# Kernel optimization log

Measured on AMD Instinct MI355X. Metric: run time of the kernel, lower is better.

## Reference

```python
import jax, jax.numpy as jnp
import numpy as np

N_HEAD = 16
HEAD_DIM = 128  # n_embd // n_head
RMS_EPS = 1.1920929e-07  # torch.finfo(float32).eps, F.rms_norm default
ROPE_BASE = 10000.0


def _rope_tables(T, head_dim, dtype=jnp.float32):
    half = head_dim // 2
    inv_freq = 1.0 / (ROPE_BASE ** (jnp.arange(half, dtype=jnp.float32) / half))
    t = jnp.arange(T, dtype=jnp.float32)
    freqs = jnp.outer(t, inv_freq)  # [T, half]
    return jnp.cos(freqs).astype(dtype), jnp.sin(freqs).astype(dtype)


def _apply_rope(x, cos, sin):
    # x: [B, T, H, D]; cos/sin: [T, D//2]
    half = x.shape[-1] // 2
    x1, x2 = x[..., :half], x[..., half:]
    c = cos[None, :, None, :]
    s = sin[None, :, None, :]
    return jnp.concatenate([x1 * c - x2 * s, x1 * s + x2 * c], axis=-1)


def _rms_norm(x):
    ms = jnp.mean(jnp.square(x), axis=-1, keepdims=True)
    return x * jax.lax.rsqrt(ms + RMS_EPS)


def setup_inputs() -> dict:
    key = jax.random.key(0)
    ks = jax.random.split(key, 5)
    B, T, E = 4, 2048, 2048
    x = jax.random.normal(ks[0], (B, T, E), dtype=jnp.float32)
    scale = 0.02
    wq = jax.random.normal(ks[1], (E, E), dtype=jnp.float32) * scale
    wk = jax.random.normal(ks[2], (E, E), dtype=jnp.float32) * scale
    wv = jax.random.normal(ks[3], (E, E), dtype=jnp.float32) * scale
    wo = jax.random.normal(ks[4], (E, E), dtype=jnp.float32) * scale
    return {"x": x, "wq": wq, "wk": wk, "wv": wv, "wo": wo}


def reference(x, wq, wk, wv, wo):
    B, T, E = x.shape
    H, D = N_HEAD, HEAD_DIM
    # QKV projections (bias-free linears)
    q = (x @ wq).reshape(B, T, H, D)
    k = (x @ wk).reshape(B, T, H, D)
    v = (x @ wv).reshape(B, T, H, D)
    # RoPE then parameter-free QK RMS norm
    cos, sin = _rope_tables(T, D, x.dtype)
    q = _rms_norm(_apply_rope(q, cos, sin))
    k = _rms_norm(_apply_rope(k, cos, sin))
    # causal SDPA
    scale = 1.0 / jnp.sqrt(jnp.asarray(D, dtype=x.dtype))
    scores = jnp.einsum('bqhd,bkhd->bhqk', q, k) * scale
    causal = jnp.tril(jnp.ones((T, T), dtype=bool))
    scores = jnp.where(causal[None, None], scores, jnp.asarray(-jnp.inf, scores.dtype))
    attn = jax.nn.softmax(scores, axis=-1)
    y = jnp.einsum('bhqk,bkhd->bqhd', attn, v).reshape(B, T, E)
    return y @ wo
```

## Files before the change

kernel.cpp:

```cpp
#include <hip/hip_runtime.h>
#include <math.h>

#define T_SEQ 2048
#define BATCH 4
#define E_DIM 2048
#define NHEAD 16
#define HDIM 128
#define RMS_EPS 1.1920929e-07f
#define NQT (T_SEQ / 128)

typedef unsigned short u16;
typedef __attribute__((ext_vector_type(8))) unsigned short u16x8;
typedef __attribute__((ext_vector_type(8))) short bf16x8;
typedef __attribute__((ext_vector_type(4))) float f32x4;

typedef const __attribute__((address_space(1))) unsigned int g_u32;
typedef __attribute__((address_space(3))) unsigned int l_u32;

static __device__ __forceinline__ u16 f2b(float f) {
  unsigned int u = __builtin_bit_cast(unsigned int, f);
  u += 0x7fffu + ((u >> 16) & 1u);
  return (u16)(u >> 16);
}
static __device__ __forceinline__ float b2f(u16 v) {
  return __builtin_bit_cast(float, ((unsigned int)v) << 16);
}

__global__ __launch_bounds__(256) void convert_f32_bf16(
    const float* __restrict__ src, u16* __restrict__ dst, int n) {
  int i = (blockIdx.x * 256 + threadIdx.x) * 4;
  if (i >= n) return;
  float4 v = *reinterpret_cast<const float4*>(src + i);
  ushort4 o;
  o.x = f2b(v.x); o.y = f2b(v.y); o.z = f2b(v.z); o.w = f2b(v.w);
  *reinterpret_cast<ushort4*>(dst + i) = o;
}

__global__ __launch_bounds__(256) void convt_w_k(
    const float* __restrict__ W, u16* __restrict__ Wt) {
  __shared__ u16 tile[64][72];
  int c0 = blockIdx.x * 64;
  int r0 = blockIdx.y * 64;
  int tid = threadIdx.x;
  int lrow = tid >> 2;
  int lcol = (tid & 3) * 16;
#pragma unroll
  for (int i = 0; i < 4; ++i) {
    float4 v = *reinterpret_cast<const float4*>(
        W + (long long)(r0 + lrow) * E_DIM + c0 + lcol + i * 4);
    tile[lrow][lcol + i * 4 + 0] = f2b(v.x);
    tile[lrow][lcol + i * 4 + 1] = f2b(v.y);
    tile[lrow][lcol + i * 4 + 2] = f2b(v.z);
    tile[lrow][lcol + i * 4 + 3] = f2b(v.w);
  }
  __syncthreads();
  int wrow = tid >> 2;
  int wcol = (tid & 3) * 16;
  u16 o[16];
#pragma unroll
  for (int i = 0; i < 16; ++i) o[i] = tile[wcol + i][wrow];
  u16* dst = Wt + (long long)(c0 + wrow) * E_DIM + r0 + wcol;
  *reinterpret_cast<u16x8*>(dst)     = *reinterpret_cast<u16x8*>(&o[0]);
  *reinterpret_cast<u16x8*>(dst + 8) = *reinterpret_cast<u16x8*>(&o[8]);
}

__global__ __launch_bounds__(256) void rope_tables_k(
    float* __restrict__ cost, float* __restrict__ sint) {
  int idx = blockIdx.x * 256 + threadIdx.x;
  int i = idx & 63, t = idx >> 6;
  double inv = pow(10000.0, -(double)i / 64.0);
  double ang = (double)t * inv;
  cost[idx] = (float)cos(ang);
  sint[idx] = (float)sin(ang);
}

__global__ __launch_bounds__(256) void rope_rms_k(
    u16* __restrict__ Qb, u16* __restrict__ Kb, const float* __restrict__ cost,
    const float* __restrict__ sint) {
  int half = gridDim.x >> 1;
  int isK = blockIdx.x >= half;
  u16* qk = isK ? Kb : Qb;
  float outscale = isK ? 1.0f : 0.08838834764831845f;
  int wave = threadIdx.x >> 6;
  int lane = threadIdx.x & 63;
  long long row = (long long)(blockIdx.x - (isK ? half : 0)) * 4 + wave;
  int th = (int)(row >> 4);
  int t = th & (T_SEQ - 1);
  u16* p = qk + row * HDIM;
  float x1 = b2f(p[lane]);
  float x2 = b2f(p[lane + 64]);
  float c = cost[t * 64 + lane];
  float s = sint[t * 64 + lane];
  float o1 = x1 * c - x2 * s;
  float o2 = x1 * s + x2 * c;
  float ss = o1 * o1 + o2 * o2;
#pragma unroll
  for (int m = 32; m >= 1; m >>= 1) ss += __shfl_xor(ss, m, 64);
  float r = rsqrtf(ss * (1.0f / 128.0f) + RMS_EPS) * outscale;
  p[lane] = f2b(o1 * r);
  p[lane + 64] = f2b(o2 * r);
}

__global__ __launch_bounds__(256) void transpose_v_k(
    const u16* __restrict__ V, u16* __restrict__ Vt) {
  __shared__ u16 tile[64][72];
  int t0 = blockIdx.x * 64, d0 = blockIdx.y * 64;
  int bh = blockIdx.z;
  int b = bh >> 4, h = bh & 15;
  int tid = threadIdx.x;
  int lrow = tid >> 3;
  int lcol = (tid & 7) * 8;
#pragma unroll
  for (int pass = 0; pass < 2; ++pass) {
    int row = lrow + pass * 32;
    const u16* src = V + ((((long long)b * T_SEQ + t0 + row) * NHEAD + h) << 7) + d0 + lcol;
    *reinterpret_cast<u16x8*>(&tile[row][lcol]) = *reinterpret_cast<const u16x8*>(src);
  }
  __syncthreads();
#pragma unroll
  for (int pass = 0; pass < 2; ++pass) {
    int drow = (tid >> 3) + pass * 32;
    int tcol = (tid & 7) * 8;
    u16x8 o;
#pragma unroll
    for (int i = 0; i < 8; ++i) o[i] = tile[tcol + i][drow];
    u16* dst = Vt + ((long long)bh * HDIM + d0 + drow) * T_SEQ + t0 + tcol;
    *reinterpret_cast<u16x8*>(dst) = o;
  }
}

__global__ __launch_bounds__(512, 2) void gemm_bt_k(
    const u16* __restrict__ A,
    const u16* __restrict__ Bt0, const u16* __restrict__ Bt1, const u16* __restrict__ Bt2,
    u16* __restrict__ C0, u16* __restrict__ C1, u16* __restrict__ C2,
    float* __restrict__ Cf, int M, int N, int K) {
  int lin = blockIdx.x + (blockIdx.y << 3) + (blockIdx.z << 8);
  int kx = lin & 7, ii = lin >> 3;
  int by = ((kx >> 1) << 3) + (ii & 7);
  int bx, bz;
  if (gridDim.z == 3) {
    int u = (kx & 1) * 12 + (ii >> 3);
    bx = u & 7; bz = u >> 3;
  } else {
    bx = ((kx & 1) << 2) + (ii >> 3);
    bz = 0;
  }
  const u16* Bt = bz == 0 ? Bt0 : (bz == 1 ? Bt1 : Bt2);
  u16* C = bz == 0 ? C0 : (bz == 1 ? C1 : C2);

  __shared__ u16 As[2][256 * 64];
  __shared__ u16 Bs[2][256 * 64];
  u16* A0 = As[0]; u16* A1 = As[1];
  u16* B0 = Bs[0]; u16* B1 = Bs[1];
  const int tid = threadIdx.x;
  const int lane = tid & 63, wave = tid >> 6;
  const int wm = wave >> 2, wn = wave & 3;
  const int m0 = by * 256, n0 = bx * 256;
  const int lr = lane & 15, lq = lane >> 4, l7 = lane & 7;
  const int NT = K >> 6;

  int rowA[2][2], rowB[2][2];
  const u16* gA[2][2];
  const u16* gB[2][2];
#pragma unroll
  for (int l = 0; l < 2; ++l) {
    int rihb = l * 64 + wave * 8;
#pragma unroll
    for (int h = 0; h < 2; ++h) {
      int ra = ((rihb >> 6) << 7) + h * 64 + (rihb & 63);
      int rb = ((rihb >> 5) << 6) + h * 32 + (rihb & 31);
      rowA[h][l] = ra;
      rowB[h][l] = rb;
      int rA = ra + (lane >> 3);
      int rB = rb + (lane >> 3);
      gA[h][l] = A + (long long)(m0 + rA) * K + ((l7 ^ (rA & 7)) * 8);
      gB[h][l] = Bt + (long long)(n0 + rB) * K + ((l7 ^ (rB & 7)) * 8);
    }
  }

  f32x4 acc[8][4] = {};
  bf16x8 aX[2][2], aY[2][2], bB[4][2];

#define GLDS(gp, lp) \
  __builtin_amdgcn_global_load_lds((g_u32*)(gp), (l_u32*)(lp), 16, 0, 0)
#define STG_A(bufp, h, off) do {                                              \
    GLDS(gA[h][0] + (off), (bufp) + rowA[h][0] * 64);                         \
    GLDS(gA[h][1] + (off), (bufp) + rowA[h][1] * 64); } while (0)
#define STG_B(bufp, h, off) do {                                              \
    GLDS(gB[h][0] + (off), (bufp) + rowB[h][0] * 64);                         \
    GLDS(gB[h][1] + (off), (bufp) + rowB[h][1] * 64); } while (0)
#define LDSA(dst, buf, mtb)                                                   \
  _Pragma("unroll") for (int mi = 0; mi < 2; ++mi)                            \
  _Pragma("unroll") for (int ks = 0; ks < 2; ++ks)                            \
    dst[mi][ks] = *reinterpret_cast<const bf16x8*>(                           \
        (buf) + (wm * 128 + ((mtb) + mi) * 16 + lr) * 64 +                    \
        ((((ks) << 2) + lq) ^ l7) * 8);
#define LDSB(dst, buf)                                                        \
  _Pragma("unroll") for (int ni = 0; ni < 4; ++ni)                            \
  _Pragma("unroll") for (int ks = 0; ks < 2; ++ks)                            \
    dst[ni][ks] = *reinterpret_cast<const bf16x8*>(                           \
        (buf) + (wn * 64 + (ni) * 16 + lr) * 64 +                             \
        ((((ks) << 2) + lq) ^ l7) * 8);
#define MFMA2(ph, a)                                                          \
  _Pragma("unroll") for (int mi = 0; mi < 2; ++mi)                            \
  _Pragma("unroll") for (int ni = 0; ni < 4; ++ni)                            \
  _Pragma("unroll") for (int ks = 0; ks < 2; ++ks)                            \
    acc[(ph) * 2 + mi][ni] = __builtin_amdgcn_mfma_f32_16x16x32_bf16(         \
        a[mi][ks], bB[ni][ks], acc[(ph) * 2 + mi][ni], 0, 0, 0);
#define SB __builtin_amdgcn_sched_barrier(0)
#define BAR __builtin_amdgcn_s_barrier()
#define VMC(n) asm volatile("s_waitcnt vmcnt(" #n ")" ::: "memory")
#define PH_MID SB; BAR; SB; __builtin_amdgcn_s_setprio(1)
#define PH_END __builtin_amdgcn_s_setprio(0); SB

  GLDS(gB[0][0], B0 + rowB[0][0] * 64); GLDS(gB[0][1], B0 + rowB[0][1] * 64);
  GLDS(gB[1][0], B0 + rowB[1][0] * 64); GLDS(gB[1][1], B0 + rowB[1][1] * 64);
  GLDS(gA[0][0], A0 + rowA[0][0] * 64); GLDS(gA[0][1], A0 + rowA[0][1] * 64);
  GLDS(gA[1][0], A0 + rowA[1][0] * 64); GLDS(gA[1][1], A0 + rowA[1][1] * 64);
  GLDS(gB[0][0] + 64, B1 + rowB[0][0] * 64); GLDS(gB[0][1] + 64, B1 + rowB[0][1] * 64);
  GLDS(gB[1][0] + 64, B1 + rowB[1][0] * 64); GLDS(gB[1][1] + 64, B1 + rowB[1][1] * 64);
  GLDS(gA[0][0] + 64, A1 + rowA[0][0] * 64); GLDS(gA[0][1] + 64, A1 + rowA[0][1] * 64);
  VMC(6);
  BAR; SB;
  LDSB(bB, B0);
  LDSA(aX, A0, 0);
  SB;

#pragma unroll 1
  for (int t = 0; t < NT; t += 2) {
    const bool nl = (t + 2 < NT);
    LDSA(aY, A0, 2);
    STG_A(A1, 1, 64);
    PH_MID; MFMA2(0, aX); PH_END;
    LDSA(aX, A0, 4);
    if (nl) { STG_B(B0, 0, 128); VMC(6); } else { VMC(4); }
    PH_MID; MFMA2(1, aY); PH_END;
    LDSA(aY, A0, 6);
    if (nl) { STG_B(B0, 1, 128); VMC(4); } else { VMC(0); }
    PH_MID; MFMA2(2, aX); PH_END;
    LDSA(aX, A1, 0);
    if (nl) STG_A(A0, 0, 128);
    PH_MID; MFMA2(3, aY);
    LDSB(bB, B1);
    PH_END;
    LDSA(aY, A1, 2);
    if (nl) STG_A(A0, 1, 128);
    PH_MID; MFMA2(0, aX); PH_END;
    LDSA(aX, A1, 4);
    if (nl) { STG_B(B1, 0, 192); VMC(6); }
    PH_MID; MFMA2(1, aY); PH_END;
    LDSA(aY, A1, 6);
    if (nl) { STG_B(B1, 1, 192); VMC(4); }
    PH_MID; MFMA2(2, aX); PH_END;
    LDSA(aX, A0, 0);
    if (nl) STG_A(A1, 0, 192);
    PH_MID; MFMA2(3, aY);
    LDSB(bB, B0);
    PH_END;
#pragma unroll
    for (int l = 0; l < 2; ++l)
#pragma unroll
      for (int h = 0; h < 2; ++h) { gA[h][l] += 128; gB[h][l] += 128; }
  }
#undef LDSA
#undef LDSB
#undef MFMA2
#undef STG_A
#undef STG_B
#undef GLDS
#undef PH_MID
#undef PH_END

#pragma unroll
  for (int mt = 0; mt < 8; ++mt)
#pragma unroll
    for (int nt = 0; nt < 4; ++nt) {
      long long col = n0 + wn * 64 + nt * 16 + lr;
#pragma unroll
      for (int r = 0; r < 4; ++r) {
        long long row = m0 + wm * 128 + mt * 16 + lq * 4 + r;
        float v = acc[mt][nt][r];
        if (Cf) Cf[row * N + col] = v;
        else C[row * N + col] = f2b(v);
      }
    }
}

__global__ __launch_bounds__(256, 3) void attn_k(
    const u16* __restrict__ Q, const u16* __restrict__ K,
    const u16* __restrict__ Vt, u16* __restrict__ Y) {
  __shared__ u16 Ks[64 * 128];
  __shared__ u16 Vs[128 * 64];
  __shared__ u16 Ps[4][32 * 72];
  __shared__ float Al[4][32];
  int lin = blockIdx.x + (blockIdx.y << 3);
  int pair = (lin >> 6);
  int bh = ((lin & 7) << 3) + ((lin >> 3) & 7);
  int b = bh >> 4, h = bh & 15;
  int tid = threadIdx.x, lane = tid & 63, wave = tid >> 6;
  int lr = lane & 15, lq = lane >> 4;

  const u16* kp[4];
  const u16* vp[4];
#pragma unroll
  for (int p = 0; p < 4; ++p) {
    int c = p * 256 + wave * 64 + lane;
    int key = c >> 4, sk = c & 15, gk = (sk - key) & 15;
    kp[p] = K + (((long long)b * T_SEQ + key) * NHEAD + h) * HDIM + gk * 8;
    int d = c >> 3, sv = c & 7, gv = (sv - d) & 7;
    vp[p] = Vt + ((long long)bh * HDIM + d) * T_SEQ + gv * 8;
  }

#pragma unroll 1
  for (int phase = 0; phase < 2; ++phase) {
    int qt = phase == 0 ? (NQT - 1 - pair) : pair;
    int qbase = qt * 128 + wave * 32;

    bf16x8 aq[2][4];
#pragma unroll
    for (int n2 = 0; n2 < 2; ++n2) {
      const u16* qp = Q + (((long long)b * T_SEQ + qbase + n2 * 16 + lr) * NHEAD + h) * HDIM;
#pragma unroll
      for (int kt = 0; kt < 4; ++kt)
        aq[n2][kt] = *reinterpret_cast<const bf16x8*>(qp + kt * 32 + lq * 8);
    }

    float m_s[2], l_s[2];
#pragma unroll
    for (int n2 = 0; n2 < 2; ++n2) { m_s[n2] = -INFINITY; l_s[n2] = 0.f; }
    f32x4 o[2][8] = {};

    int niter = 2 * qt + 2;
    for (int j = 0; j < niter; ++j) {
      __syncthreads();
#pragma unroll
      for (int p = 0; p < 4; ++p) {
        __builtin_amdgcn_global_load_lds(
            (g_u32*)(kp[p] + (long long)j * 64 * NHEAD * HDIM),
            (l_u32*)(Ks + p * 2048 + wave * 512), 16, 0, 0);
        __builtin_amdgcn_global_load_lds(
            (g_u32*)(vp[p] + j * 64),
            (l_u32*)(Vs + p * 2048 + wave * 512), 16, 0, 0);
      }
      __syncthreads();

      f32x4 s[4][2];
#pragma unroll
      for (int mt = 0; mt < 4; ++mt) {
        int key = mt * 16 + lr;
        bf16x8 ak[4];
#pragma unroll
        for (int kt = 0; kt < 4; ++kt) {
          int slot = (kt * 4 + lq + key) & 15;
          ak[kt] = *reinterpret_cast<const bf16x8*>(&Ks[key * 128 + slot * 8]);
        }
#pragma unroll
        for (int n2 = 0; n2 < 2; ++n2) {
          f32x4 acc = {};
#pragma unroll
          for (int kt = 0; kt < 4; ++kt)
            acc = __builtin_amdgcn_mfma_f32_16x16x32_bf16(ak[kt], aq[n2][kt], acc, 0, 0, 0);
          s[mt][n2] = acc;
        }
      }

      if (j >= 2 * qt) {
#pragma unroll
        for (int mt = 0; mt < 4; ++mt)
#pragma unroll
          for (int n2 = 0; n2 < 2; ++n2) {
            int q = qbase + n2 * 16 + lr;
#pragma unroll
            for (int r = 0; r < 4; ++r) {
              int key = j * 64 + mt * 16 + lq * 4 + r;
              if (key > q) s[mt][n2][r] = -INFINITY;
            }
          }
      }

      float alpha[2];
#pragma unroll
      for (int n2 = 0; n2 < 2; ++n2) {
        float mx = s[0][n2][0];
#pragma unroll
        for (int mt = 0; mt < 4; ++mt)
#pragma unroll
          for (int r = 0; r < 4; ++r) mx = fmaxf(mx, s[mt][n2][r]);
        mx = fmaxf(mx, __shfl_xor(mx, 16, 64));
        mx = fmaxf(mx, __shfl_xor(mx, 32, 64));
        float mn = fmaxf(m_s[n2], mx);
        alpha[n2] = __expf(m_s[n2] - mn);
        m_s[n2] = mn;
        float sum = 0.f;
        int q = n2 * 16 + lr;
#pragma unroll
        for (int mt = 0; mt < 4; ++mt) {
          ushort4 pk;
          float p0 = __expf(s[mt][n2][0] - mn);
          float p1 = __expf(s[mt][n2][1] - mn);
          float p2 = __expf(s[mt][n2][2] - mn);
          float p3 = __expf(s[mt][n2][3] - mn);
          sum += (p0 + p1) + (p2 + p3);
          pk.x = f2b(p0); pk.y = f2b(p1); pk.z = f2b(p2); pk.w = f2b(p3);
          *reinterpret_cast<ushort4*>(&Ps[wave][q * 72 + mt * 16 + lq * 4]) = pk;
        }
        sum += __shfl_xor(sum, 16, 64);
        sum += __shfl_xor(sum, 32, 64);
        l_s[n2] = l_s[n2] * alpha[n2] + sum;
      }

      if (lq == 0) {
        Al[wave][lr] = alpha[0];
        Al[wave][16 + lr] = alpha[1];
      }
#pragma unroll
      for (int q2 = 0; q2 < 2; ++q2) {
        f32x4 av = *reinterpret_cast<const f32x4*>(&Al[wave][q2 * 16 + lq * 4]);
#pragma unroll
        for (int r = 0; r < 4; ++r)
#pragma unroll
          for (int dt = 0; dt < 8; ++dt) o[q2][dt][r] *= av[r];
      }

#pragma unroll
      for (int kh = 0; kh < 2; ++kh) {
        bf16x8 ap[2];
#pragma unroll
        for (int q2 = 0; q2 < 2; ++q2)
          ap[q2] = *reinterpret_cast<const bf16x8*>(
              &Ps[wave][(q2 * 16 + lr) * 72 + kh * 32 + lq * 8]);
#pragma unroll
        for (int dt = 0; dt < 8; ++dt) {
          int d = dt * 16 + lr;
          int slot = (kh * 4 + lq + d) & 7;
          bf16x8 bv = *reinterpret_cast<const bf16x8*>(&Vs[d * 64 + slot * 8]);
#pragma unroll
          for (int q2 = 0; q2 < 2; ++q2)
            o[q2][dt] = __builtin_amdgcn_mfma_f32_16x16x32_bf16(ap[q2], bv, o[q2][dt], 0, 0, 0);
        }
      }
    }

    if (lq == 0) {
      Al[wave][lr] = l_s[0];
      Al[wave][16 + lr] = l_s[1];
    }
#pragma unroll
    for (int q2 = 0; q2 < 2; ++q2) {
      f32x4 lv = *reinterpret_cast<const f32x4*>(&Al[wave][q2 * 16 + lq * 4]);
#pragma unroll
      for (int r = 0; r < 4; ++r) {
        float inv = 1.0f / lv[r];
        int q = qbase + q2 * 16 + lq * 4 + r;
        u16* yp = Y + (((long long)b * T_SEQ + q) * NHEAD + h) * HDIM;
#pragma unroll
        for (int dt = 0; dt < 8; ++dt)
          yp[dt * 16 + lr] = f2b(o[q2][dt][r] * inv);
      }
    }
  }
}

extern "C" void kernel_launch(void* const* d_in, const int* in_sizes, int n_in,
                              void* d_out, int out_size, void* d_ws, size_t ws_size,
                              hipStream_t stream) {
  (void)in_sizes; (void)n_in; (void)out_size; (void)ws_size;
  const float* x  = (const float*)d_in[0];
  const float* wq = (const float*)d_in[1];
  const float* wk = (const float*)d_in[2];
  const float* wv = (const float*)d_in[3];
  const float* wo = (const float*)d_in[4];
  float* out = (float*)d_out;

  char* ws = (char*)d_ws;
  size_t off = 0;
  auto alloc = [&](size_t bytes) {
    char* p = ws + off;
    off += (bytes + 255) & ~(size_t)255;
    return p;
  };
  const size_t NTOK = (size_t)BATCH * T_SEQ;
  const size_t XE = NTOK * E_DIM;
  const size_t WE = (size_t)E_DIM * E_DIM;

  u16* xb  = (u16*)alloc(XE * 2);
  u16* wqt = (u16*)alloc(WE * 2);
  u16* wkt = (u16*)alloc(WE * 2);
  u16* wvt = (u16*)alloc(WE * 2);
  u16* wot = (u16*)alloc(WE * 2);
  u16* Qb  = (u16*)alloc(XE * 2);
  u16* Kb  = (u16*)alloc(XE * 2);
  u16* Vb  = (u16*)alloc(XE * 2);
  u16* Vt  = (u16*)alloc(XE * 2);
  u16* Yb  = (u16*)alloc(XE * 2);
  float* cost = (float*)alloc((size_t)T_SEQ * 64 * 4);
  float* sint = (float*)alloc((size_t)T_SEQ * 64 * 4);

  convert_f32_bf16<<<XE / 1024, 256, 0, stream>>>(x, xb, (int)XE);
  dim3 gw(E_DIM / 64, E_DIM / 64);
  convt_w_k<<<gw, 256, 0, stream>>>(wq, wqt);
  convt_w_k<<<gw, 256, 0, stream>>>(wk, wkt);
  convt_w_k<<<gw, 256, 0, stream>>>(wv, wvt);
  convt_w_k<<<gw, 256, 0, stream>>>(wo, wot);
  rope_tables_k<<<(T_SEQ * 64) / 256, 256, 0, stream>>>(cost, sint);

  dim3 gq(E_DIM / 256, NTOK / 256, 3);
  gemm_bt_k<<<gq, 512, 0, stream>>>(xb, wqt, wkt, wvt, Qb, Kb, Vb, nullptr,
                                    (int)NTOK, E_DIM, E_DIM);

  rope_rms_k<<<(unsigned)(NTOK * NHEAD / 4) * 2, 256, 0, stream>>>(Qb, Kb, cost, sint);

  dim3 gt(T_SEQ / 64, HDIM / 64, BATCH * NHEAD);
  transpose_v_k<<<gt, 256, 0, stream>>>(Vb, Vt);

  dim3 ga(NQT / 2, BATCH * NHEAD);
  attn_k<<<ga, 256, 0, stream>>>(Qb, Kb, Vt, Yb);

  dim3 go(E_DIM / 256, NTOK / 256, 1);
  gemm_bt_k<<<go, 512, 0, stream>>>(Yb, wot, wot, wot, nullptr, nullptr, nullptr, out,
                                    (int)NTOK, E_DIM, E_DIM);
}
```

Before: 618.9 us.

## Double-buffer K tiles and prefetch V in attention loop

Restructures the attention kernel's K/V staging into a software pipeline. K now uses two LDS buffers, so the next-next K tile is loaded asynchronously while the current one is consumed, and the next V tile is issued right after the PV MFMAs, with explicit vmcnt waits and barriers. The aim is to hide global-load latency that was previously exposed by the load-then-sync pattern. This costs more LDS, which lowers the launch-bounds occupancy hint from 3 to 2 blocks, and adds extra barriers per iteration.

```diff
diff --git a/kernel.cpp b/kernel.cpp
--- a/kernel.cpp
+++ b/kernel.cpp
@@ -267,7 +267,6 @@
 #undef MFMA2
 #undef STG_A
 #undef STG_B
-#undef GLDS
 #undef PH_MID
 #undef PH_END
 
@@ -286,10 +285,10 @@
     }
 }
 
-__global__ __launch_bounds__(256, 3) void attn_k(
+__global__ __launch_bounds__(256, 2) void attn_k(
     const u16* __restrict__ Q, const u16* __restrict__ K,
     const u16* __restrict__ Vt, u16* __restrict__ Y) {
-  __shared__ u16 Ks[64 * 128];
+  __shared__ u16 Ks2[2][64 * 128];
   __shared__ u16 Vs[128 * 64];
   __shared__ u16 Ps[4][32 * 72];
   __shared__ float Al[4][32];
@@ -310,11 +309,24 @@
     int d = c >> 3, sv = c & 7, gv = (sv - d) & 7;
     vp[p] = Vt + ((long long)bh * HDIM + d) * T_SEQ + gv * 8;
   }
+  const long long KSTRIDE = (long long)64 * NHEAD * HDIM;
+
+#define AGL(gp, lp) \
+  __builtin_amdgcn_global_load_lds((g_u32*)(gp), (l_u32*)(lp), 16, 0, 0)
+#define AVMC(n) asm volatile("s_waitcnt vmcnt(" #n ")" ::: "memory")
+#define STG_K(j, buf) do { _Pragma("unroll")                                  \
+    for (int p = 0; p < 4; ++p)                                               \
+      AGL(kp[p] + (long long)(j) * KSTRIDE,                                   \
+          Ks2[buf] + p * 2048 + wave * 512); } while (0)
+#define STG_V(j) do { _Pragma("unroll")                                       \
+    for (int p = 0; p < 4; ++p)                                               \
+      AGL(vp[p] + (j) * 64, Vs + p * 2048 + wave * 512); } while (0)
 
 #pragma unroll 1
   for (int phase = 0; phase < 2; ++phase) {
     int qt = phase == 0 ? (NQT - 1 - pair) : pair;
     int qbase = qt * 128 + wave * 32;
+    int niter = 2 * qt + 2;
 
     bf16x8 aq[2][4];
 #pragma unroll
@@ -330,19 +342,15 @@
     for (int n2 = 0; n2 < 2; ++n2) { m_s[n2] = -INFINITY; l_s[n2] = 0.f; }
     f32x4 o[2][8] = {};
 
-    int niter = 2 * qt + 2;
+    STG_K(0, 0);
+    AVMC(0);
+    __builtin_amdgcn_s_barrier();
+    STG_V(0);
+    STG_K(1, 1);
+
+#pragma unroll 1
     for (int j = 0; j < niter; ++j) {
-      __syncthreads();
-#pragma unroll
-      for (int p = 0; p < 4; ++p) {
-        __builtin_amdgcn_global_load_lds(
-            (g_u32*)(kp[p] + (long long)j * 64 * NHEAD * HDIM),
-            (l_u32*)(Ks + p * 2048 + wave * 512), 16, 0, 0);
-        __builtin_amdgcn_global_load_lds(
-            (g_u32*)(vp[p] + j * 64),
-            (l_u32*)(Vs + p * 2048 + wave * 512), 16, 0, 0);
-      }
-      __syncthreads();
+      const u16* Kb = Ks2[j & 1];
 
       f32x4 s[4][2];
 #pragma unroll
@@ -352,7 +360,7 @@
 #pragma unroll
         for (int kt = 0; kt < 4; ++kt) {
           int slot = (kt * 4 + lq + key) & 15;
-          ak[kt] = *reinterpret_cast<const bf16x8*>(&Ks[key * 128 + slot * 8]);
+          ak[kt] = *reinterpret_cast<const bf16x8*>(&Kb[key * 128 + slot * 8]);
         }
 #pragma unroll
         for (int n2 = 0; n2 < 2; ++n2) {
@@ -422,6 +430,9 @@
           for (int dt = 0; dt < 8; ++dt) o[q2][dt][r] *= av[r];
       }
 
+      if (j + 1 < niter) { AVMC(4); } else { AVMC(0); }
+      __builtin_amdgcn_s_barrier();
+
 #pragma unroll
       for (int kh = 0; kh < 2; ++kh) {
         bf16x8 ap[2];
@@ -439,6 +450,18 @@
             o[q2][dt] = __builtin_amdgcn_mfma_f32_16x16x32_bf16(ap[q2], bv, o[q2][dt], 0, 0, 0);
         }
       }
+
+      if (j + 1 < niter) {
+        __builtin_amdgcn_s_barrier();
+        STG_V(j + 1);
+        if (j + 2 < niter) {
+          STG_K(j + 2, j & 1);
+          AVMC(8);
+        } else {
+          AVMC(4);
+        }
+        __builtin_amdgcn_s_barrier();
+      }
     }
 
     if (lq == 0) {
@@ -459,6 +482,10 @@
       }
     }
   }
+#undef STG_K
+#undef STG_V
+#undef AGL
+#undef AVMC
 }
 
 extern "C" void kernel_launch(void* const* d_in, const int* in_sizes, int n_in,
```

Result: faster. 571.5 us (-7.7%).
